# Kernel optimization log

Measured on AMD Instinct MI355X. Metric: run time of the kernel, lower is better.

The kernel has to match this reference:

```python
import jax, jax.numpy as jnp
import numpy as np

R_MAX = 5.0
AVG_NEI = 16.0
NB = 8
L_OF_LM = np.repeat(np.arange(4), [1, 3, 5, 7])  # lm index -> l, 16 components for l_max=3


def real_sph(u):
    # real spherical harmonics up to l=3, component normalization; u: [E,3] unit vectors
    x, y, z = u[:, 0], u[:, 1], u[:, 2]
    x2, y2, z2 = x * x, y * y, z * z
    return jnp.stack([
        jnp.ones_like(x),
        1.7320508 * x, 1.7320508 * y, 1.7320508 * z,
        3.8729833 * x * y, 3.8729833 * y * z,
        1.1180340 * (3.0 * z2 - 1.0),
        3.8729833 * x * z, 1.9364917 * (x2 - y2),
        2.0916500 * y * (3.0 * x2 - y2), 10.246951 * x * y * z,
        1.6201852 * y * (5.0 * z2 - 1.0), 1.3228757 * z * (5.0 * z2 - 3.0),
        1.6201852 * x * (5.0 * z2 - 1.0), 5.1234753 * z * (x2 - y2),
        2.0916500 * x * (x2 - 3.0 * y2),
    ], axis=-1)


def radial_embed(r):
    # Bessel basis * polynomial (p=5) envelope, as in MACE RadialEmbeddingBlock
    n = jnp.arange(1, NB + 1, dtype=r.dtype)
    bess = jnp.sqrt(2.0 / R_MAX) * jnp.sin(n * jnp.pi * r[:, None] / R_MAX) / (r[:, None] + 1e-8)
    p = 5.0
    t = jnp.clip(r / R_MAX, 0.0, 1.0)
    env = 1.0 - 0.5 * (p + 1) * (p + 2) * t**p + p * (p + 2) * t**(p + 1) - 0.5 * p * (p + 1) * t**(p + 2)
    return bess * env[:, None]


def interaction(feats, Y, R, senders, receivers, Wu, Wd, num_nodes):
    # feats: [N,C,Din] (Din = sum of (2l+1) over input l-blocks); Y: [E,16]; R: [E,C,12] radial path weights
    n_lin = Wu.shape[0]
    up = jnp.concatenate([
        jnp.einsum('ncm,cd->ndm', feats[:, :, l * l:(l + 1) * (l + 1)], Wu[l])
        for l in range(n_lin)], axis=-1)
    hs = up[senders]  # gather sender features [E,C,Din]
    R0, R1, R2 = R[..., 0:4], R[..., 4:8], R[..., 8:12]
    # CG path (0, l_sh) -> l_sh : scalar feature times Y_l
    msg = R0[:, :, L_OF_LM] * hs[:, :, 0:1] * Y[:, None, :]  # [E,C,16]
    for l in range(1, n_lin):
        sl = slice(l * l, (l + 1) * (l + 1))
        # CG path (l, 0) -> l
        msg = msg.at[:, :, sl].add(R1[:, :, l:l + 1] * hs[:, :, sl] * Y[:, None, 0:1])
        # CG path (l, l) -> 0 : invariant dot product
        msg = msg.at[:, :, 0].add(R2[:, :, l] * jnp.sum(hs[:, :, sl] * Y[:, None, sl], axis=-1))
    agg = jnp.zeros((num_nodes, msg.shape[1], msg.shape[2]), msg.dtype).at[receivers].add(msg) / AVG_NEI
    return jnp.einsum('ncm,mcd->ndm', agg, Wd[L_OF_LM])  # per-l linear down


def setup_inputs() -> dict:
    key = jax.random.key(0)
    ks = jax.random.split(key, 18)
    N, E, C, S = 10000, 160000, 64, 10
    f32 = jnp.float32
    rn = lambda k, shape, scale: jax.random.normal(k, shape, f32) * scale
    return {
        'edge_vectors': rn(ks[0], (E, 3), 1.5),
        'node_embed': rn(ks[1], (S, C), 0.3),
        'rw1': rn(ks[2], (2, NB, 64), 1.0 / np.sqrt(NB)),
        'rw2': rn(ks[3], (2, 64, C * 12), 1.0 / np.sqrt(64)),
        'lu0': rn(ks[4], (1, C, C), 1.0 / np.sqrt(C)),
        'lu1': rn(ks[5], (2, C, C), 1.0 / np.sqrt(C)),
        'ld': rn(ks[6], (2, 4, C, C), 1.0 / np.sqrt(C)),
        'sel_w': rn(ks[7], (S, 4, C, C), 1.0 / np.sqrt(C)),
        'prod_w0': rn(ks[8], (S, C, C), 1.0 / np.sqrt(C)),
        'prod_w1': rn(ks[9], (S, C, C), 1.0 / np.sqrt(C)),
        'res_w': rn(ks[10], (S, C, C), 1.0 / np.sqrt(C)),
        'read0': rn(ks[11], (C, 1), 1.0 / np.sqrt(C)),
        'mlp_w1': rn(ks[12], (C, 32), 1.0 / np.sqrt(C)),
        'mlp_w2': rn(ks[13], (32, 1), 1.0 / np.sqrt(32)),
        'node_species': jax.random.randint(ks[14], (N,), 0, S),
        'senders': jax.random.randint(ks[15], (E,), 0, N),
        'receivers': jax.random.randint(ks[16], (E,), 0, N),
    }


def reference(edge_vectors, node_embed, rw1, rw2, lu0, lu1, ld, sel_w, prod_w0,
              prod_w1, res_w, read0, mlp_w1, mlp_w2, node_species, senders, receivers):
    N = node_species.shape[0]
    C = node_embed.shape[1]
    r = jnp.linalg.norm(edge_vectors, axis=-1)
    u = edge_vectors / (r[:, None] + 1e-8)
    Y = real_sph(u)                      # [E,16]
    rb = radial_embed(r)                 # [E,8]
    R_all = [(jax.nn.silu(rb @ rw1[i]) @ rw2[i]).reshape(-1, C, 12) for i in range(2)]
    # ---- layer 0 (selector_tp, not last) ----
    f = node_embed[node_species][:, :, None]               # [N,C,1] scalar embed
    f = interaction(f, Y, R_all[0], senders, receivers, lu0, ld[0], N)  # [N,C,16]
    blocks = []
    for l in range(4):  # species-dependent selector TP (per-l channel mixing)
        sl = slice(l * l, (l + 1) * (l + 1))
        blocks.append(jnp.einsum('ncm,ncd->ndm', f[:, :, sl], sel_w[node_species, l]))
    f = jnp.concatenate(blocks, axis=-1)
    # product basis (correlation 3 polynomial in invariant channel), target C x (0e+1o)
    s = f[:, :, 0]
    f1 = jnp.einsum('ncm,ncd->ndm', f[:, :, :4] * (1.0 + s + s * s)[:, :, None], prod_w0[node_species])
    out0 = f1[:, :, 0] @ read0           # linear readout head  [N,1]
    # ---- layer 1 (last, residual) ----
    res = jnp.einsum('nc,ncd->nd', f1[:, :, 0], res_w[node_species])
    g = interaction(f1, Y, R_all[1], senders, receivers, lu1, ld[1], N)  # [N,C,16]
    inv = g[:, :, 0] + jnp.sum(g[:, :, 1:] ** 2, axis=-1)  # invariants from all l blocks
    f2 = jnp.einsum('nc,ncd->nd', inv + inv * inv, prod_w1[node_species]) + res
    out1 = jax.nn.silu(f2 @ mlp_w1) @ mlp_w2  # nonlinear readout  [N,1]
    # stack heads (axis=2) then layers (axis=1): [N, num_interactions, num_heads, 1]
    return jnp.stack([out0, out1], axis=1)[:, :, None, :]
```

## Files before the change

### kernel.cpp

```cpp
#include <hip/hip_runtime.h>
#include <math.h>


#define WAVE_SZ 64

typedef _Float16 half8 __attribute__((ext_vector_type(8)));
typedef _Float16 half4v __attribute__((ext_vector_type(4)));
typedef float f32x4 __attribute__((ext_vector_type(4)));

__device__ __forceinline__ float silu_f(float x) { return x / (1.0f + expf(-x)); }

__device__ __forceinline__ float reduce64(float v) {
#pragma unroll
  for (int off = 32; off > 0; off >>= 1) v += __shfl_xor(v, off, WAVE_SZ);
  return v;
}

__device__ __forceinline__ void compute_Y(float x, float y, float z, float* Y) {
  float x2 = x * x, y2 = y * y, z2 = z * z;
  Y[0] = 1.0f;
  Y[1] = 1.7320508f * x;
  Y[2] = 1.7320508f * y;
  Y[3] = 1.7320508f * z;
  Y[4] = 3.8729833f * x * y;
  Y[5] = 3.8729833f * y * z;
  Y[6] = 1.118034f * (3.0f * z2 - 1.0f);
  Y[7] = 3.8729833f * x * z;
  Y[8] = 1.9364917f * (x2 - y2);
  Y[9] = 2.09165f * y * (3.0f * x2 - y2);
  Y[10] = 10.246951f * x * y * z;
  Y[11] = 1.6201852f * y * (5.0f * z2 - 1.0f);
  Y[12] = 1.3228757f * z * (5.0f * z2 - 3.0f);
  Y[13] = 1.6201852f * x * (5.0f * z2 - 1.0f);
  Y[14] = 5.1234753f * z * (x2 - y2);
  Y[15] = 2.09165f * x * (x2 - 3.0f * y2);
}

__device__ __forceinline__ void compute_rb(float r, float inv_r, float* rb) {
  float t = fminf(r * 0.2f, 1.0f);
  float t2 = t * t;
  float t5 = t2 * t2 * t;
  float env = 1.0f + t5 * (-21.0f + t * (35.0f - 15.0f * t));
  float th = 0.62831853f * r;
  float s1 = sinf(th), c1 = cosf(th);
  float c2 = 2.0f * c1;
  float sprev = 0.0f, scur = s1;
  float coef = 0.63245553f * inv_r * env;
#pragma unroll
  for (int k = 0; k < 8; k++) {
    rb[k] = coef * scur;
    float snxt = c2 * scur - sprev;
    sprev = scur;
    scur = snxt;
  }
}

__global__ __launch_bounds__(256) void k_hist(const int* __restrict__ receivers,
                                              int* __restrict__ cnt, int E) {
  int e = blockIdx.x * 256 + threadIdx.x;
  if (e < E) atomicAdd(&cnt[receivers[e]], 1);
}

__global__ __launch_bounds__(256) void k_scan(const int* __restrict__ deg,
                                              int* __restrict__ row_start,
                                              int* __restrict__ cursor, int N) {
  __shared__ int part[256];
  int t = threadIdx.x;
  int K = (N + 255) / 256;
  int lo = t * K, hi = min(lo + K, N);
  int s = 0;
  for (int i = lo; i < hi; i++) s += deg[i];
  part[t] = s;
  __syncthreads();
  for (int d = 1; d < 256; d <<= 1) {
    int v = (t >= d) ? part[t - d] : 0;
    __syncthreads();
    part[t] += v;
    __syncthreads();
  }
  int run = (t == 0) ? 0 : part[t - 1];
  for (int i = lo; i < hi; i++) {
    int di = deg[i];
    row_start[i] = run;
    cursor[i] = run;
    run += di;
  }
  if (t == 255) row_start[N] = part[255];
}

__global__ __launch_bounds__(256) void k_scatter(const int* __restrict__ receivers,
                                                 const int* __restrict__ senders,
                                                 int* __restrict__ cursor,
                                                 int* __restrict__ perm,
                                                 int* __restrict__ rsort,
                                                 int* __restrict__ ssort, int E) {
  int e = blockIdx.x * 256 + threadIdx.x;
  if (e < E) {
    int r = receivers[e];
    int pos = atomicAdd(&cursor[r], 1);
    perm[pos] = e;
    rsort[pos] = r;
    ssort[pos] = senders[e];
  }
}

__global__ __launch_bounds__(256) void k_pack(const float* __restrict__ rw2,
                                              _Float16* __restrict__ b1t,
                                              _Float16* __restrict__ b2t) {
  int idx = blockIdx.x * 256 + threadIdx.x;
  if (idx < 8192) {
    int n = idx >> 6, k = idx & 63;
    int c = n >> 1, j = n & 1;
    b1t[idx] = (_Float16)rw2[k * 768 + c * 12 + j];
  } else if (idx < 32768) {
    int i2 = idx - 8192;
    int n = i2 >> 6, k = i2 & 63;
    int c = n / 6, j = n - c * 6;
    int col = (j < 4) ? j : ((j == 4) ? 5 : 9);
    b2t[i2] = (_Float16)rw2[49152 + k * 768 + c * 12 + col];
  }
}

__global__ __launch_bounds__(256) void k_up0(const float* __restrict__ embed,
                                             const float* __restrict__ lu0,
                                             const int* __restrict__ species,
                                             float* __restrict__ up0, int N) {
  int wave = threadIdx.x >> 6, lane = threadIdx.x & 63;
  int n = (blockIdx.x << 2) + wave;
  if (n >= N) return;
  int sp = species[n];
  const float* er = embed + sp * 64;
  float acc = 0.0f;
#pragma unroll 8
  for (int c = 0; c < 64; c++) acc += er[c] * lu0[c * 64 + lane];
  up0[(size_t)n * 64 + lane] = acc;
}

__global__ __launch_bounds__(256) void k_geom(const float* __restrict__ ev,
                                              const float* __restrict__ rw1,
                                              const int* __restrict__ perm,
                                              _Float16* __restrict__ hid0,
                                              _Float16* __restrict__ hid1,
                                              float* __restrict__ Ysort,
                                              int* __restrict__ rsort,
                                              int* __restrict__ ssort,
                                              int E, int EPAD) {
  int wave = threadIdx.x >> 6, lane = threadIdx.x & 63;
  int j = blockIdx.x * 4 + wave;
  if (j >= EPAD) return;
  if (j >= E) {
    hid0[(size_t)j * 64 + lane] = (_Float16)0.0f;
    hid1[(size_t)j * 64 + lane] = (_Float16)0.0f;
    if (lane == 0) { rsort[j] = -1; ssort[j] = 0; }
    if (lane < 16) Ysort[(size_t)j * 16 + lane] = 0.0f;
    return;
  }
  int e = perm[j];
  float vx = ev[e * 3 + 0], vy = ev[e * 3 + 1], vz = ev[e * 3 + 2];
  float r = sqrtf(vx * vx + vy * vy + vz * vz);
  float inv_r = 1.0f / (r + 1e-8f);
  float Y[16];
  compute_Y(vx * inv_r, vy * inv_r, vz * inv_r, Y);
  float rb[8];
  compute_rb(r, inv_r, rb);

  float h0 = 0.0f, h1 = 0.0f;
#pragma unroll
  for (int k = 0; k < 8; k++) {
    h0 += rb[k] * rw1[k * 64 + lane];
    h1 += rb[k] * rw1[512 + k * 64 + lane];
  }
  hid0[(size_t)j * 64 + lane] = (_Float16)silu_f(h0);
  hid1[(size_t)j * 64 + lane] = (_Float16)silu_f(h1);

  float yv = Y[0];
#pragma unroll
  for (int m = 1; m < 16; m++) yv = (lane == m) ? Y[m] : yv;
  if (lane < 16) Ysort[(size_t)j * 16 + lane] = yv;
}

__global__ __launch_bounds__(256) void k_fagg1(const _Float16* __restrict__ hid,
                                               const _Float16* __restrict__ bt,
                                               const float* __restrict__ Ysort,
                                               const float* __restrict__ up0,
                                               const int* __restrict__ ssort,
                                               const int* __restrict__ rsort,
                                               float* __restrict__ agg1c, int E) {
  __shared__ _Float16 __attribute__((aligned(16))) lds[4][16 * 128];
  int wave = threadIdx.x >> 6, lane = threadIdx.x & 63;
  int q = lane >> 4, mr = lane & 15;
  _Float16* L = lds[wave];
  int j0 = __builtin_amdgcn_readfirstlane((blockIdx.x * 4 + wave) * 16);

  int rs[16], ss[16];
#pragma unroll
  for (int t = 0; t < 16; t++) {
    rs[t] = rsort[j0 + t];
    ss[t] = ssort[j0 + t];
  }
  float hsv[16];
#pragma unroll
  for (int t = 0; t < 16; t++) hsv[t] = up0[((size_t)ss[t] << 6) + lane];

  const half8* Ap = (const half8*)(hid + (size_t)(j0 + mr) * 64 + q * 8);
  half8 a0 = Ap[0];
  half8 a1 = Ap[4];
  const _Float16* bp = bt + (size_t)mr * 64 + q * 8;
#pragma unroll
  for (int T = 0; T < 8; T++) {
    half8 b0 = *(const half8*)(bp + T * 1024);
    half8 b1 = *(const half8*)(bp + T * 1024 + 32);
    f32x4 acc = {0.f, 0.f, 0.f, 0.f};
    acc = __builtin_amdgcn_mfma_f32_16x16x32_f16(a0, b0, acc, 0, 0, 0);
    acc = __builtin_amdgcn_mfma_f32_16x16x32_f16(a1, b1, acc, 0, 0, 0);
#pragma unroll
    for (int r = 0; r < 4; r++)
      L[(q * 4 + r) * 128 + T * 16 + mr] = (_Float16)acc[r];
  }

  float accm[4] = {0.f, 0.f, 0.f, 0.f};
  int cur_r = (j0 < E) ? rs[0] : -1;

#pragma unroll
  for (int t = 0; t < 16; t++) {
    int j = j0 + t;
    bool ok = (j < E);
    int rr = ok ? rs[t] : -2;
    if (rr != cur_r) {
      if (cur_r >= 0) {
        float* base = agg1c + ((size_t)cur_r << 8) + lane;
#pragma unroll
        for (int m = 0; m < 4; m++) atomicAdd(base + (m << 6), accm[m]);
      }
#pragma unroll
      for (int m = 0; m < 4; m++) accm[m] = 0.0f;
      cur_r = rr;
    }
    if (ok) {
      float hs0 = hsv[t];
      const _Float16* Rr = L + t * 128 + lane * 2;
      float p0 = (float)Rr[0] * hs0;
      float p1 = (float)Rr[1] * hs0;
      float4 Ya = *(const float4*)(Ysort + (size_t)j * 16);
      accm[0] += p0;
      accm[1] += p1 * Ya.y;
      accm[2] += p1 * Ya.z;
      accm[3] += p1 * Ya.w;
    }
  }
  if (cur_r >= 0) {
    float* base = agg1c + ((size_t)cur_r << 8) + lane;
#pragma unroll
    for (int m = 0; m < 4; m++) atomicAdd(base + (m << 6), accm[m]);
  }
}

__global__ __launch_bounds__(256) void k_fagg2(const _Float16* __restrict__ hid,
                                               const _Float16* __restrict__ bt,
                                               const float* __restrict__ Ysort,
                                               const _Float16* __restrict__ up1,
                                               const int* __restrict__ ssort,
                                               const int* __restrict__ rsort,
                                               float* __restrict__ agg, int E) {
  __shared__ _Float16 __attribute__((aligned(16))) lds[4][16 * 384];
  int wave = threadIdx.x >> 6, lane = threadIdx.x & 63;
  int q = lane >> 4, mr = lane & 15;
  _Float16* L = lds[wave];
  int j0 = __builtin_amdgcn_readfirstlane((blockIdx.x * 4 + wave) * 16);

  int rs[16], ss[16];
#pragma unroll
  for (int t = 0; t < 16; t++) {
    rs[t] = rsort[j0 + t];
    ss[t] = ssort[j0 + t];
  }
  half4v hA[8];
#pragma unroll
  for (int t = 0; t < 8; t++)
    hA[t] = *(const half4v*)(up1 + ((size_t)ss[t] << 8) + lane * 4);

  const half8* Ap = (const half8*)(hid + (size_t)(j0 + mr) * 64 + q * 8);
  half8 a0 = Ap[0];
  half8 a1 = Ap[4];
  const _Float16* bp = bt + (size_t)mr * 64 + q * 8;
#pragma unroll
  for (int T = 0; T < 24; T++) {
    half8 b0 = *(const half8*)(bp + T * 1024);
    half8 b1 = *(const half8*)(bp + T * 1024 + 32);
    f32x4 acc = {0.f, 0.f, 0.f, 0.f};
    acc = __builtin_amdgcn_mfma_f32_16x16x32_f16(a0, b0, acc, 0, 0, 0);
    acc = __builtin_amdgcn_mfma_f32_16x16x32_f16(a1, b1, acc, 0, 0, 0);
#pragma unroll
    for (int r = 0; r < 4; r++)
      L[(q * 4 + r) * 384 + T * 16 + mr] = (_Float16)acc[r];
  }

  half4v hB[8];
#pragma unroll
  for (int t = 0; t < 8; t++)
    hB[t] = *(const half4v*)(up1 + ((size_t)ss[8 + t] << 8) + lane * 4);

  float accm[16];
#pragma unroll
  for (int m = 0; m < 16; m++) accm[m] = 0.0f;
  int cur_r = (j0 < E) ? rs[0] : -1;

#pragma unroll
  for (int t = 0; t < 16; t++) {
    int j = j0 + t;
    bool ok = (j < E);
    int rr = ok ? rs[t] : -2;
    if (rr != cur_r) {
      if (cur_r >= 0) {
        float* base = agg + ((size_t)cur_r << 10) + lane;
#pragma unroll
        for (int m = 0; m < 16; m++) atomicAdd(base + (m << 6), accm[m]);
      }
#pragma unroll
      for (int m = 0; m < 16; m++) accm[m] = 0.0f;
      cur_r = rr;
    }
    if (ok) {
      half4v hs = (t < 8) ? hA[t & 7] : hB[t & 7];
      float hs0 = (float)hs.x, hs1 = (float)hs.y;
      float hs2 = (float)hs.z, hs3 = (float)hs.w;
      const _Float16* Rr = L + t * 384 + lane * 6;
      float R0 = (float)Rr[0], R1v = (float)Rr[1];
      float R2v = (float)Rr[2], R3v = (float)Rr[3];
      float c5 = (float)Rr[4], c9 = (float)Rr[5];
      float q0 = R0 * hs0, q1 = R1v * hs0, q2 = R2v * hs0, q3 = R3v * hs0;
      const float* Yj = Ysort + (size_t)j * 16;
      float4 Ya = *(const float4*)(Yj);
      float4 Yb = *(const float4*)(Yj + 4);
      float4 Yc = *(const float4*)(Yj + 8);
      float4 Yd = *(const float4*)(Yj + 12);
      accm[0] += q0 + c9 * (hs1 * Ya.y + hs2 * Ya.z + hs3 * Ya.w);
      accm[1] += q1 * Ya.y + c5 * hs1;
      accm[2] += q1 * Ya.z + c5 * hs2;
      accm[3] += q1 * Ya.w + c5 * hs3;
      accm[4] += q2 * Yb.x;
      accm[5] += q2 * Yb.y;
      accm[6] += q2 * Yb.z;
      accm[7] += q2 * Yb.w;
      accm[8] += q2 * Yc.x;
      accm[9] += q3 * Yc.y;
      accm[10] += q3 * Yc.z;
      accm[11] += q3 * Yc.w;
      accm[12] += q3 * Yd.x;
      accm[13] += q3 * Yd.y;
      accm[14] += q3 * Yd.z;
      accm[15] += q3 * Yd.w;
    }
  }
  if (cur_r >= 0) {
    float* base = agg + ((size_t)cur_r << 10) + lane;
#pragma unroll
    for (int m = 0; m < 16; m++) atomicAdd(base + (m << 6), accm[m]);
  }
}

__global__ __launch_bounds__(64) void k_node1(const float* __restrict__ agg1c,
                                              const float* __restrict__ ld0,
                                              const float* __restrict__ sel_w,
                                              const float* __restrict__ pw0,
                                              const float* __restrict__ res_w,
                                              const float* __restrict__ lu1,
                                              const float* __restrict__ read0,
                                              const int* __restrict__ species,
                                              float* __restrict__ out,
                                              float* __restrict__ res,
                                              _Float16* __restrict__ up1, int N) {
  int n = blockIdx.x, d = threadIdx.x;
  int sp = species[n];
  __shared__ float sA[256], sB[256];

  const float* ag = agg1c + ((size_t)n << 8);
#pragma unroll
  for (int m = 0; m < 4; m++) sA[m * 64 + d] = ag[(m << 6) + d] * 0.0625f;
  __syncthreads();

  float fr[4] = {0.f, 0.f, 0.f, 0.f};
  {
    const float* W0 = ld0 + d;
    const float* W1 = ld0 + 4096 + d;
#pragma unroll 8
    for (int c = 0; c < 64; c++) {
      float w0 = W0[c * 64], w1 = W1[c * 64];
      fr[0] += sA[c] * w0;
      fr[1] += sA[64 + c] * w1;
      fr[2] += sA[128 + c] * w1;
      fr[3] += sA[192 + c] * w1;
    }
  }
#pragma unroll
  for (int m = 0; m < 4; m++) sB[m * 64 + d] = fr[m];
  __syncthreads();

  float f2r[4] = {0.f, 0.f, 0.f, 0.f};
  {
    const float* W0 = sel_w + ((size_t)(sp * 4) << 12) + d;
    const float* W1 = sel_w + ((size_t)(sp * 4 + 1) << 12) + d;
#pragma unroll 8
    for (int c = 0; c < 64; c++) {
      float w0 = W0[c * 64], w1 = W1[c * 64];
      f2r[0] += sB[c] * w0;
      f2r[1] += sB[64 + c] * w1;
      f2r[2] += sB[128 + c] * w1;
      f2r[3] += sB[192 + c] * w1;
    }
  }
  float s0 = f2r[0];
  float tt = 1.0f + s0 + s0 * s0;
#pragma unroll
  for (int m = 0; m < 4; m++) sA[m * 64 + d] = f2r[m] * tt;
  __syncthreads();

  float f1r[4] = {0.f, 0.f, 0.f, 0.f};
  {
    const float* W = pw0 + ((size_t)sp << 12) + d;
#pragma unroll 8
    for (int c = 0; c < 64; c++) {
      float w = W[c * 64];
#pragma unroll
      for (int m = 0; m < 4; m++) f1r[m] += sA[m * 64 + c] * w;
    }
  }
#pragma unroll
  for (int m = 0; m < 4; m++) sB[m * 64 + d] = f1r[m];
  __syncthreads();

  float v = reduce64(f1r[0] * read0[d]);
  if (d == 0) out[2 * n] = v;

  float u0;
  {
    const float* Wr = res_w + ((size_t)sp << 12) + d;
    const float* Wu = lu1 + d;
    float a = 0.0f, b = 0.0f;
#pragma unroll 8
    for (int c = 0; c < 64; c++) {
      float fv = sB[c];
      a += fv * Wr[c * 64];
      b += fv * Wu[c * 64];
    }
    res[((size_t)n << 6) + d] = a;
    u0 = b;
  }
  {
    const float* Wu = lu1 + 4096 + d;
    float a1 = 0.f, a2 = 0.f, a3 = 0.f;
#pragma unroll 8
    for (int c = 0; c < 64; c++) {
      float w = Wu[c * 64];
      a1 += sB[64 + c] * w;
      a2 += sB[128 + c] * w;
      a3 += sB[192 + c] * w;
    }
    half4v uu;
    uu.x = (_Float16)u0;
    uu.y = (_Float16)a1;
    uu.z = (_Float16)a2;
    uu.w = (_Float16)a3;
    *(half4v*)(up1 + ((size_t)n << 8) + d * 4) = uu;
  }
}

__global__ __launch_bounds__(64) void k_node2(const float* __restrict__ agg1,
                                              const float* __restrict__ ld1,
                                              const float* __restrict__ pw1,
                                              const float* __restrict__ res,
                                              const float* __restrict__ mlp_w1,
                                              const float* __restrict__ mlp_w2,
                                              const int* __restrict__ species,
                                              float* __restrict__ out, int N) {
  int n = blockIdx.x, d = threadIdx.x;
  int sp = species[n];
  __shared__ float sA[1024];

  const float* ag = agg1 + ((size_t)n << 10);
#pragma unroll
  for (int m = 0; m < 16; m++) sA[m * 64 + d] = ag[(m << 6) + d] * 0.0625f;
  __syncthreads();

  float g[16];
#pragma unroll
  for (int m = 0; m < 16; m++) g[m] = 0.0f;
#pragma unroll
  for (int l = 0; l < 4; l++) {
    int m0 = l * l, m1 = (l + 1) * (l + 1);
    const float* W = ld1 + l * 4096 + d;
#pragma unroll 8
    for (int c = 0; c < 64; c++) {
      float w = W[c * 64];
      for (int m = m0; m < m1; m++) g[m] += sA[m * 64 + c] * w;
    }
  }
  float inv = g[0];
#pragma unroll
  for (int m = 1; m < 16; m++) inv += g[m] * g[m];
  float qv = inv + inv * inv;
  __syncthreads();
  sA[d] = qv;
  __syncthreads();

  float a = res[((size_t)n << 6) + d];
  {
    const float* W = pw1 + ((size_t)sp << 12) + d;
#pragma unroll 8
    for (int c = 0; c < 64; c++) a += sA[c] * W[c * 64];
  }
  sA[64 + d] = a;
  __syncthreads();

  float val = 0.0f;
  if (d < 32) {
    float h = 0.0f;
#pragma unroll 8
    for (int c = 0; c < 64; c++) h += sA[64 + c] * mlp_w1[c * 32 + d];
    val = silu_f(h) * mlp_w2[d];
  }
  val = reduce64(val);
  if (d == 0) out[2 * n + 1] = val;
}

extern "C" void kernel_launch(void* const* d_in, const int* in_sizes, int n_in,
                              void* d_out, int out_size, void* d_ws, size_t ws_size,
                              hipStream_t stream) {
  const float* ev      = (const float*)d_in[0];
  const float* embed   = (const float*)d_in[1];
  const float* rw1     = (const float*)d_in[2];
  const float* rw2     = (const float*)d_in[3];
  const float* lu0     = (const float*)d_in[4];
  const float* lu1     = (const float*)d_in[5];
  const float* ld      = (const float*)d_in[6];
  const float* sel_w   = (const float*)d_in[7];
  const float* pw0     = (const float*)d_in[8];
  const float* pw1     = (const float*)d_in[9];
  const float* res_w   = (const float*)d_in[10];
  const float* read0   = (const float*)d_in[11];
  const float* mlp_w1  = (const float*)d_in[12];
  const float* mlp_w2  = (const float*)d_in[13];
  const int* species   = (const int*)d_in[14];
  const int* senders   = (const int*)d_in[15];
  const int* receivers = (const int*)d_in[16];
  float* out = (float*)d_out;

  int N = in_sizes[14];
  int E = in_sizes[15];
  int EPAD = ((E + 63) / 64) * 64;

  float* ws = (float*)d_ws;
  size_t o = 0;
  float* agg   = ws + o;  o += (size_t)N * 1024;
  float* agg1c = ws + o;  o += (size_t)N * 256;
  float* up0   = ws + o;  o += (size_t)N * 64;
  _Float16* up1 = (_Float16*)(ws + o); o += (size_t)N * 128;
  float* resb  = ws + o;  o += (size_t)N * 64;
  _Float16* b1t  = (_Float16*)(ws + o); o += 4096;
  _Float16* b2t  = (_Float16*)(ws + o); o += 12288;
  _Float16* hid0 = (_Float16*)(ws + o); o += (size_t)EPAD * 32;
  _Float16* hid1 = (_Float16*)(ws + o); o += (size_t)EPAD * 32;
  float* Ysort = ws + o;  o += (size_t)EPAD * 16;
  int* row_start = (int*)(ws + o); o += (size_t)N + 1;
  int* cursor    = (int*)(ws + o); o += (size_t)N;
  int* perm      = (int*)(ws + o); o += (size_t)E;
  int* rsort     = (int*)(ws + o); o += (size_t)EPAD;
  int* ssort     = (int*)(ws + o); o += (size_t)EPAD;

  hipMemsetAsync(agg, 0, (size_t)N * 1280 * sizeof(float), stream);
  hipMemsetAsync(cursor, 0, (size_t)N * sizeof(int), stream);

  k_hist<<<(E + 255) / 256, 256, 0, stream>>>(receivers, cursor, E);
  k_scan<<<1, 256, 0, stream>>>(cursor, row_start, cursor, N);
  k_scatter<<<(E + 255) / 256, 256, 0, stream>>>(receivers, senders, cursor,
                                                 perm, rsort, ssort, E);

  k_pack<<<128, 256, 0, stream>>>(rw2, b1t, b2t);
  k_up0<<<(N + 3) / 4, 256, 0, stream>>>(embed, lu0, species, up0, N);
  k_geom<<<EPAD / 4, 256, 0, stream>>>(ev, rw1, perm, hid0, hid1, Ysort,
                                       rsort, ssort, E, EPAD);

  int fblocks = EPAD / 64;
  k_fagg1<<<fblocks, 256, 0, stream>>>(hid0, b1t, Ysort, up0, ssort, rsort,
                                       agg1c, E);
  k_node1<<<N, 64, 0, stream>>>(agg1c, ld, sel_w, pw0, res_w, lu1, read0,
                                species, out, resb, up1, N);
  k_fagg2<<<fblocks, 256, 0, stream>>>(hid1, b2t, Ysort, up1, ssort, rsort,
                                       agg, E);
  k_node2<<<N, 64, 0, stream>>>(agg, ld + 16384, pw1, resb, mlp_w1, mlp_w2,
                                species, out, N);
}
```

Measured before the change: 418.4 us.

## Batch node2 over 16 nodes and use fp16 MFMA for down-projection

k_node2 now handles 16 nodes per 256-thread block instead of one node per 64-thread block. The per-l down-projection (ld1) runs as 16x16x32 fp16 MFMAs against a transposed fp16 copy of ld1 packed in k_pack. The product and MLP readouts are reused across nodes through padded LDS. k_fagg2 also gets a min-blocks-per-CU launch bound of 3. Aggregated features are cast to fp16 before the MFMA, which lowers precision.

```diff
diff --git a/kernel.cpp b/kernel.cpp
--- a/kernel.cpp
+++ b/kernel.cpp
@@ -2,7 +2,7 @@
 #include <math.h>
 
 
-#define WAVE_SZ 64
+#define LANES 64
 
 typedef _Float16 half8 __attribute__((ext_vector_type(8)));
 typedef _Float16 half4v __attribute__((ext_vector_type(4)));
@@ -12,8 +12,12 @@
 
 __device__ __forceinline__ float reduce64(float v) {
 #pragma unroll
-  for (int off = 32; off > 0; off >>= 1) v += __shfl_xor(v, off, WAVE_SZ);
+  for (int off = 32; off > 0; off >>= 1) v += __shfl_xor(v, off, LANES);
   return v;
+}
+
+__device__ __forceinline__ int l_of_m(int m) {
+  return (m == 0) ? 0 : ((m < 4) ? 1 : ((m < 9) ? 2 : 3));
 }
 
 __device__ __forceinline__ void compute_Y(float x, float y, float z, float* Y) {
@@ -105,8 +109,10 @@
 }
 
 __global__ __launch_bounds__(256) void k_pack(const float* __restrict__ rw2,
+                                              const float* __restrict__ ldw,
                                               _Float16* __restrict__ b1t,
-                                              _Float16* __restrict__ b2t) {
+                                              _Float16* __restrict__ b2t,
+                                              _Float16* __restrict__ ld1t) {
   int idx = blockIdx.x * 256 + threadIdx.x;
   if (idx < 8192) {
     int n = idx >> 6, k = idx & 63;
@@ -118,6 +124,12 @@
     int c = n / 6, j = n - c * 6;
     int col = (j < 4) ? j : ((j == 4) ? 5 : 9);
     b2t[i2] = (_Float16)rw2[49152 + k * 768 + c * 12 + col];
+  } else if (idx < 49152) {
+    int i3 = idx - 32768;
+    int l = i3 >> 12;
+    int rem = i3 & 4095;
+    int dd = rem >> 6, cc = rem & 63;
+    ld1t[i3] = (_Float16)ldw[16384 + (l << 12) + (cc << 6) + dd];
   }
 }
 
@@ -255,13 +267,13 @@
   }
 }
 
-__global__ __launch_bounds__(256) void k_fagg2(const _Float16* __restrict__ hid,
-                                               const _Float16* __restrict__ bt,
-                                               const float* __restrict__ Ysort,
-                                               const _Float16* __restrict__ up1,
-                                               const int* __restrict__ ssort,
-                                               const int* __restrict__ rsort,
-                                               float* __restrict__ agg, int E) {
+__global__ __launch_bounds__(256, 3) void k_fagg2(const _Float16* __restrict__ hid,
+                                                  const _Float16* __restrict__ bt,
+                                                  const float* __restrict__ Ysort,
+                                                  const _Float16* __restrict__ up1,
+                                                  const int* __restrict__ ssort,
+                                                  const int* __restrict__ rsort,
+                                                  float* __restrict__ agg, int E) {
   __shared__ _Float16 __attribute__((aligned(16))) lds[4][16 * 384];
   int wave = threadIdx.x >> 6, lane = threadIdx.x & 63;
   int q = lane >> 4, mr = lane & 15;
@@ -465,62 +477,84 @@
   }
 }
 
-__global__ __launch_bounds__(64) void k_node2(const float* __restrict__ agg1,
-                                              const float* __restrict__ ld1,
-                                              const float* __restrict__ pw1,
-                                              const float* __restrict__ res,
-                                              const float* __restrict__ mlp_w1,
-                                              const float* __restrict__ mlp_w2,
-                                              const int* __restrict__ species,
-                                              float* __restrict__ out, int N) {
-  int n = blockIdx.x, d = threadIdx.x;
-  int sp = species[n];
-  __shared__ float sA[1024];
-
-  const float* ag = agg1 + ((size_t)n << 10);
-#pragma unroll
-  for (int m = 0; m < 16; m++) sA[m * 64 + d] = ag[(m << 6) + d] * 0.0625f;
+__global__ __launch_bounds__(256) void k_node2(const float* __restrict__ agg1,
+                                               const _Float16* __restrict__ ld1t,
+                                               const float* __restrict__ pw1,
+                                               const float* __restrict__ res,
+                                               const float* __restrict__ mlp_w1,
+                                               const float* __restrict__ mlp_w2,
+                                               const int* __restrict__ species,
+                                               float* __restrict__ out, int N) {
+  __shared__ float sq[16 * 65];
+  __shared__ float sf[16 * 65];
+  int tid = threadIdx.x;
+  int wave = tid >> 6, lane = tid & 63;
+  int q = lane >> 4, mr = lane & 15;
+  int nb = blockIdx.x * 16;
+
+  int arow = min(nb + mr, N - 1);
+  const float* Arow = agg1 + ((size_t)arow << 10);
+
+  float inv[4] = {0.f, 0.f, 0.f, 0.f};
+#pragma unroll
+  for (int m = 0; m < 16; m++) {
+    int l = l_of_m(m);
+    const float* ap = Arow + (m << 6) + q * 8;
+    half8 a0, a1;
+#pragma unroll
+    for (int i = 0; i < 8; i++) {
+      a0[i] = (_Float16)(ap[i] * 0.0625f);
+      a1[i] = (_Float16)(ap[32 + i] * 0.0625f);
+    }
+    const _Float16* bp = ld1t + (l << 12) + ((wave * 16 + mr) << 6) + q * 8;
+    half8 b0 = *(const half8*)(bp);
+    half8 b1 = *(const half8*)(bp + 32);
+    f32x4 acc = {0.f, 0.f, 0.f, 0.f};
+    acc = __builtin_amdgcn_mfma_f32_16x16x32_f16(a0, b0, acc, 0, 0, 0);
+    acc = __builtin_amdgcn_mfma_f32_16x16x32_f16(a1, b1, acc, 0, 0, 0);
+    if (m == 0) {
+#pragma unroll
+      for (int r = 0; r < 4; r++) inv[r] += acc[r];
+    } else {
+#pragma unroll
+      for (int r = 0; r < 4; r++) inv[r] += acc[r] * acc[r];
+    }
+  }
+#pragma unroll
+  for (int r = 0; r < 4; r++) {
+    float iv = inv[r];
+    sq[(q * 4 + r) * 65 + wave * 16 + mr] = iv + iv * iv;
+  }
   __syncthreads();
 
-  float g[16];
-#pragma unroll
-  for (int m = 0; m < 16; m++) g[m] = 0.0f;
-#pragma unroll
-  for (int l = 0; l < 4; l++) {
-    int m0 = l * l, m1 = (l + 1) * (l + 1);
-    const float* W = ld1 + l * 4096 + d;
-#pragma unroll 8
-    for (int c = 0; c < 64; c++) {
-      float w = W[c * 64];
-      for (int m = m0; m < m1; m++) g[m] += sA[m * 64 + c] * w;
-    }
-  }
-  float inv = g[0];
-#pragma unroll
-  for (int m = 1; m < 16; m++) inv += g[m] * g[m];
-  float qv = inv + inv * inv;
+  int d = lane;
+#pragma unroll
+  for (int g = 0; g < 4; g++) {
+    int nl = wave + 4 * g;
+    int n = nb + nl;
+    int nc = min(n, N - 1);
+    int sp = species[nc];
+    float a = res[((size_t)nc << 6) + d];
+    const float* W = pw1 + ((size_t)sp << 12) + d;
+#pragma unroll 8
+    for (int c = 0; c < 64; c++) a += sq[nl * 65 + c] * W[c * 64];
+    sf[nl * 65 + d] = a;
+  }
   __syncthreads();
-  sA[d] = qv;
-  __syncthreads();
-
-  float a = res[((size_t)n << 6) + d];
-  {
-    const float* W = pw1 + ((size_t)sp << 12) + d;
-#pragma unroll 8
-    for (int c = 0; c < 64; c++) a += sA[c] * W[c * 64];
-  }
-  sA[64 + d] = a;
-  __syncthreads();
-
-  float val = 0.0f;
-  if (d < 32) {
-    float h = 0.0f;
-#pragma unroll 8
-    for (int c = 0; c < 64; c++) h += sA[64 + c] * mlp_w1[c * 32 + d];
-    val = silu_f(h) * mlp_w2[d];
-  }
-  val = reduce64(val);
-  if (d == 0) out[2 * n + 1] = val;
+
+#pragma unroll
+  for (int p = 0; p < 2; p++) {
+    int nl = wave * 2 + (lane >> 5) + p * 8;
+    int n = nb + nl;
+    int h = lane & 31;
+    float hh = 0.f;
+#pragma unroll 8
+    for (int c = 0; c < 64; c++) hh += sf[nl * 65 + c] * mlp_w1[c * 32 + h];
+    float val = silu_f(hh) * mlp_w2[h];
+#pragma unroll
+    for (int off = 16; off > 0; off >>= 1) val += __shfl_xor(val, off, 64);
+    if (h == 0 && n < N) out[2 * n + 1] = val;
+  }
 }
 
 extern "C" void kernel_launch(void* const* d_in, const int* in_sizes, int n_in,
@@ -558,6 +592,7 @@
   float* resb  = ws + o;  o += (size_t)N * 64;
   _Float16* b1t  = (_Float16*)(ws + o); o += 4096;
   _Float16* b2t  = (_Float16*)(ws + o); o += 12288;
+  _Float16* ld1t = (_Float16*)(ws + o); o += 8192;
   _Float16* hid0 = (_Float16*)(ws + o); o += (size_t)EPAD * 32;
   _Float16* hid1 = (_Float16*)(ws + o); o += (size_t)EPAD * 32;
   float* Ysort = ws + o;  o += (size_t)EPAD * 16;
@@ -575,7 +610,7 @@
   k_scatter<<<(E + 255) / 256, 256, 0, stream>>>(receivers, senders, cursor,
                                                  perm, rsort, ssort, E);
 
-  k_pack<<<128, 256, 0, stream>>>(rw2, b1t, b2t);
+  k_pack<<<192, 256, 0, stream>>>(rw2, ld, b1t, b2t, ld1t);
   k_up0<<<(N + 3) / 4, 256, 0, stream>>>(embed, lu0, species, up0, N);
   k_geom<<<EPAD / 4, 256, 0, stream>>>(ev, rw1, perm, hid0, hid1, Ysort,
                                        rsort, ssort, E, EPAD);
@@ -587,6 +622,6 @@
                                 species, out, resb, up1, N);
   k_fagg2<<<fblocks, 256, 0, stream>>>(hid1, b2t, Ysort, up1, ssort, rsort,
                                        agg, E);
-  k_node2<<<N, 64, 0, stream>>>(agg, ld + 16384, pw1, resb, mlp_w1, mlp_w2,
-                                species, out, N);
-}
+  k_node2<<<(N + 15) / 16, 256, 0, stream>>>(agg, ld1t, pw1, resb, mlp_w1,
+                                             mlp_w2, species, out, N);
+}
```

Measured after the change: 408.6 us. 1.02x faster.
